# Kernel tuning notes

Hardware: AMD Instinct MI355X
Metric: run time of the kernel (lower is better)

Reference implementation:

```python
import jax, jax.numpy as jnp
import numpy as np

FRAMES = 31
FFT_LEN = 2048


def setup_inputs() -> dict:
    key = jax.random.key(0)
    ks = jax.random.split(key, 7)
    B = 1024
    x = jax.random.normal(ks[0], (B, FRAMES * FFT_LEN), dtype=jnp.float32)
    # torch nn.Linear params: weight [out, in], bias [out]
    def lin(k, fan_in, fan_out):
        bound = 1.0 / np.sqrt(fan_in)
        kw, kb = jax.random.split(k)
        W = jax.random.uniform(kw, (fan_out, fan_in), minval=-bound, maxval=bound, dtype=jnp.float32)
        b = jax.random.uniform(kb, (fan_out,), minval=-bound, maxval=bound, dtype=jnp.float32)
        return W, b
    W1, b1 = lin(ks[1], FFT_LEN, 256)
    W2, b2 = lin(ks[2], 256, 256)
    W3, b3 = lin(ks[3], 256, 1)
    return {"x": x, "W1": W1, "b1": b1, "W2": W2, "b2": b2, "W3": W3, "b3": b3}


def reference(x, W1, b1, W2, b2, W3, b3):
    B = x.shape[0]
    # flatten, take first 31*2048 elements, reshape, batched FFT along last axis
    xf = x.reshape(B, -1)[:, : FRAMES * FFT_LEN].reshape(B, FRAMES, FFT_LEN)
    spec = jnp.fft.fftn(xf, axes=(-1,))          # [B, 31, 2048] complex64
    spec_mean = jnp.mean(spec, axis=1)            # [B, 2048] complex64
    h = spec_mean.real.astype(jnp.float32)        # torch .type(FloatTensor) keeps real part
    h = jax.nn.relu(h @ W1.T + b1)
    h = jax.nn.relu(h @ W2.T + b2)
    out = jax.nn.sigmoid(h @ W3.T + b3)           # [B, 1]
    return out
```

## Files before the change

### kernel.cpp

```cpp
#include <hip/hip_runtime.h>
#include <math.h>

#define B 1024
#define FRAMES 31
#define NFFT 2048
#define NH 256
#define TWO_PI 6.28318530717958647692f

#define KSPLIT 16
#define KRANGE (NFFT / KSPLIT)
#define BT 32
#define JP 260
#define HP 36

__global__ __launch_bounds__(256) void k_mean_fft(const float* __restrict__ x,
                                                  float* __restrict__ h) {
    __shared__ float re[NFFT];
    __shared__ float im[NFFT];
    __shared__ float ct[NFFT];
    const int tid = threadIdx.x;
    const int b = blockIdx.x;
    const float* xr = x + (size_t)b * (FRAMES * NFFT);

#pragma unroll
    for (int s = 0; s < 8; ++s) {
        int i = tid + (s << 8);
        ct[i] = cosf(TWO_PI * (float)i / (float)NFFT);
    }

    float acc[8];
#pragma unroll
    for (int s = 0; s < 8; ++s) acc[s] = 0.f;
    for (int f = 0; f < FRAMES; ++f) {
        const float* fr = xr + f * NFFT;
#pragma unroll
        for (int s = 0; s < 8; ++s) acc[s] += fr[tid + (s << 8)];
    }
    const float inv = 1.0f / (float)FRAMES;
#pragma unroll
    for (int s = 0; s < 8; ++s) {
        int n = tid + (s << 8);
        int rv = __brev((unsigned)n) >> 21;
        re[rv] = acc[s] * inv;
        im[rv] = 0.f;
    }
    __syncthreads();

    for (int stage = 1; stage <= 11; ++stage) {
        const int half = 1 << (stage - 1);
        const int tsh = 11 - stage;
#pragma unroll
        for (int s = 0; s < 4; ++s) {
            int idx = tid + (s << 8);
            int j = idx & (half - 1);
            int base = ((idx >> (stage - 1)) << stage) + j;
            int ti = j << tsh;
            float wr = ct[ti];
            float wi = -ct[(ti + 1536) & (NFFT - 1)];
            float ar = re[base], ai = im[base];
            float br = re[base + half], bi = im[base + half];
            float tr = wr * br - wi * bi;
            float tq = wr * bi + wi * br;
            re[base] = ar + tr;
            im[base] = ai + tq;
            re[base + half] = ar - tr;
            im[base + half] = ai - tq;
        }
        __syncthreads();
    }

    float* hr = h + (size_t)b * NFFT;
#pragma unroll
    for (int s = 0; s < 8; ++s)
        hr[tid + (s << 8)] = re[tid + (s << 8)];
}

__global__ __launch_bounds__(256) void k_gemm1(const float* __restrict__ h,
                                               const float* __restrict__ W1,
                                               float* __restrict__ yp) {
    __shared__ float W1s[32 * JP];
    __shared__ float hs[32 * HP];
    const int tid = threadIdx.x;
    const int b0 = blockIdx.x * BT;
    const int kb0 = blockIdx.y * KRANGE;

    const int j0 = (tid & 63) * 4;
    const int bo = (tid >> 6) * 8;

    float acc[8][4];
#pragma unroll
    for (int i = 0; i < 8; ++i)
#pragma unroll
        for (int q = 0; q < 4; ++q) acc[i][q] = 0.f;

    for (int kc = 0; kc < KRANGE; kc += 32) {
        const int kb = kb0 + kc;
#pragma unroll
        for (int s = 0; s < 8; ++s) {
            int f = tid + (s << 8);
            int j = f >> 3;
            int k4 = f & 7;
            float4 v = *(const float4*)(W1 + (size_t)j * NFFT + kb + k4 * 4);
            W1s[(k4 * 4 + 0) * JP + j] = v.x;
            W1s[(k4 * 4 + 1) * JP + j] = v.y;
            W1s[(k4 * 4 + 2) * JP + j] = v.z;
            W1s[(k4 * 4 + 3) * JP + j] = v.w;
        }
        {
            int bb = tid >> 3;
            int k4 = tid & 7;
            float4 v = *(const float4*)(h + (size_t)(b0 + bb) * NFFT + kb + k4 * 4);
            hs[(k4 * 4 + 0) * HP + bb] = v.x;
            hs[(k4 * 4 + 1) * HP + bb] = v.y;
            hs[(k4 * 4 + 2) * HP + bb] = v.z;
            hs[(k4 * 4 + 3) * HP + bb] = v.w;
        }
        __syncthreads();

#pragma unroll 8
        for (int k = 0; k < 32; ++k) {
            float4 w = *(const float4*)&W1s[k * JP + j0];
            float4 hA = *(const float4*)&hs[k * HP + bo];
            float4 hB = *(const float4*)&hs[k * HP + bo + 4];
            acc[0][0] = fmaf(hA.x, w.x, acc[0][0]); acc[0][1] = fmaf(hA.x, w.y, acc[0][1]);
            acc[0][2] = fmaf(hA.x, w.z, acc[0][2]); acc[0][3] = fmaf(hA.x, w.w, acc[0][3]);
            acc[1][0] = fmaf(hA.y, w.x, acc[1][0]); acc[1][1] = fmaf(hA.y, w.y, acc[1][1]);
            acc[1][2] = fmaf(hA.y, w.z, acc[1][2]); acc[1][3] = fmaf(hA.y, w.w, acc[1][3]);
            acc[2][0] = fmaf(hA.z, w.x, acc[2][0]); acc[2][1] = fmaf(hA.z, w.y, acc[2][1]);
            acc[2][2] = fmaf(hA.z, w.z, acc[2][2]); acc[2][3] = fmaf(hA.z, w.w, acc[2][3]);
            acc[3][0] = fmaf(hA.w, w.x, acc[3][0]); acc[3][1] = fmaf(hA.w, w.y, acc[3][1]);
            acc[3][2] = fmaf(hA.w, w.z, acc[3][2]); acc[3][3] = fmaf(hA.w, w.w, acc[3][3]);
            acc[4][0] = fmaf(hB.x, w.x, acc[4][0]); acc[4][1] = fmaf(hB.x, w.y, acc[4][1]);
            acc[4][2] = fmaf(hB.x, w.z, acc[4][2]); acc[4][3] = fmaf(hB.x, w.w, acc[4][3]);
            acc[5][0] = fmaf(hB.y, w.x, acc[5][0]); acc[5][1] = fmaf(hB.y, w.y, acc[5][1]);
            acc[5][2] = fmaf(hB.y, w.z, acc[5][2]); acc[5][3] = fmaf(hB.y, w.w, acc[5][3]);
            acc[6][0] = fmaf(hB.z, w.x, acc[6][0]); acc[6][1] = fmaf(hB.z, w.y, acc[6][1]);
            acc[6][2] = fmaf(hB.z, w.z, acc[6][2]); acc[6][3] = fmaf(hB.z, w.w, acc[6][3]);
            acc[7][0] = fmaf(hB.w, w.x, acc[7][0]); acc[7][1] = fmaf(hB.w, w.y, acc[7][1]);
            acc[7][2] = fmaf(hB.w, w.z, acc[7][2]); acc[7][3] = fmaf(hB.w, w.w, acc[7][3]);
        }
        __syncthreads();
    }

    float* yo = yp + (size_t)blockIdx.y * (B * NH);
#pragma unroll
    for (int i = 0; i < 8; ++i) {
        float4 v = make_float4(acc[i][0], acc[i][1], acc[i][2], acc[i][3]);
        *(float4*)(yo + (size_t)(b0 + bo + i) * NH + j0) = v;
    }
}

__global__ __launch_bounds__(256) void k_reduce_relu(const float* __restrict__ yp,
                                                     const float* __restrict__ b1,
                                                     float* __restrict__ y1) {
    int f = blockIdx.x * 256 + threadIdx.x;
    const float4* p = (const float4*)yp;
    float4 a = p[f];
#pragma unroll
    for (int s = 1; s < KSPLIT; ++s) {
        float4 v = p[f + s * (B * NH / 4)];
        a.x += v.x; a.y += v.y; a.z += v.z; a.w += v.w;
    }
    float4 bb = ((const float4*)b1)[f & 63];
    a.x = fmaxf(a.x + bb.x, 0.f);
    a.y = fmaxf(a.y + bb.y, 0.f);
    a.z = fmaxf(a.z + bb.z, 0.f);
    a.w = fmaxf(a.w + bb.w, 0.f);
    ((float4*)y1)[f] = a;
}

__global__ __launch_bounds__(256) void k_head(const float* __restrict__ y1,
                                              const float* __restrict__ W2,
                                              const float* __restrict__ b2,
                                              const float* __restrict__ W3,
                                              const float* __restrict__ b3,
                                              float* __restrict__ out) {
    __shared__ float ys[4 * NH];
    __shared__ float red[4 * NH];
    const int tid = threadIdx.x;
    const int b0 = blockIdx.x * 4;
    ((float4*)ys)[tid] = ((const float4*)(y1 + (size_t)b0 * NH))[tid];
    __syncthreads();

    const float4* w2 = (const float4*)(W2 + (size_t)tid * NH);
    float a0 = 0.f, a1 = 0.f, a2 = 0.f, a3 = 0.f;
#pragma unroll 8
    for (int n4 = 0; n4 < NH / 4; ++n4) {
        float4 w = w2[n4];
        float4 v0 = ((const float4*)ys)[n4];
        float4 v1 = ((const float4*)ys)[64 + n4];
        float4 v2 = ((const float4*)ys)[128 + n4];
        float4 v3 = ((const float4*)ys)[192 + n4];
        a0 = fmaf(w.x, v0.x, a0); a0 = fmaf(w.y, v0.y, a0);
        a0 = fmaf(w.z, v0.z, a0); a0 = fmaf(w.w, v0.w, a0);
        a1 = fmaf(w.x, v1.x, a1); a1 = fmaf(w.y, v1.y, a1);
        a1 = fmaf(w.z, v1.z, a1); a1 = fmaf(w.w, v1.w, a1);
        a2 = fmaf(w.x, v2.x, a2); a2 = fmaf(w.y, v2.y, a2);
        a2 = fmaf(w.z, v2.z, a2); a2 = fmaf(w.w, v2.w, a2);
        a3 = fmaf(w.x, v3.x, a3); a3 = fmaf(w.y, v3.y, a3);
        a3 = fmaf(w.z, v3.z, a3); a3 = fmaf(w.w, v3.w, a3);
    }
    float w3 = W3[tid];
    float bb = b2[tid];
    red[tid]       = fmaxf(a0 + bb, 0.f) * w3;
    red[256 + tid] = fmaxf(a1 + bb, 0.f) * w3;
    red[512 + tid] = fmaxf(a2 + bb, 0.f) * w3;
    red[768 + tid] = fmaxf(a3 + bb, 0.f) * w3;
    __syncthreads();
    for (int s = 128; s > 0; s >>= 1) {
        if (tid < s) {
#pragma unroll
            for (int q = 0; q < 4; ++q)
                red[q * 256 + tid] += red[q * 256 + tid + s];
        }
        __syncthreads();
    }
    if (tid < 4)
        out[b0 + tid] = 1.f / (1.f + expf(-(red[tid * 256] + b3[0])));
}

extern "C" void kernel_launch(void* const* d_in, const int* in_sizes, int n_in,
                              void* d_out, int out_size, void* d_ws, size_t ws_size,
                              hipStream_t stream) {
    const float* x  = (const float*)d_in[0];
    const float* W1 = (const float*)d_in[1];
    const float* b1 = (const float*)d_in[2];
    const float* W2 = (const float*)d_in[3];
    const float* b2 = (const float*)d_in[4];
    const float* W3 = (const float*)d_in[5];
    const float* b3 = (const float*)d_in[6];
    float* out = (float*)d_out;

    char* ws = (char*)d_ws;
    float* h  = (float*)(ws);
    float* yp = (float*)(ws + (8u  << 20));
    float* y1 = (float*)(ws + (24u << 20));

    hipLaunchKernelGGL(k_mean_fft,    dim3(B),       dim3(256), 0, stream, x, h);
    hipLaunchKernelGGL(k_gemm1,       dim3(32, 16),  dim3(256), 0, stream, h, W1, yp);
    hipLaunchKernelGGL(k_reduce_relu, dim3(256),     dim3(256), 0, stream, yp, b1, y1);
    hipLaunchKernelGGL(k_head,        dim3(256),     dim3(256), 0, stream, y1, W2, b2, W3, b3, out);
}
```

Measured before the change: 426.9 us.

## Use real-FFT symmetry to halve FFT size and fold W1 columns

Exploits Hermitian symmetry of the real input's spectrum: a 1024-point complex FFT with a post-twiddle step produces the real part for bins 0..1023. W1 columns k and N-k are summed into a folded weight matrix, halving the GEMM K dimension, and the Nyquist bin is added separately in the tail. The reduce/ReLU kernel is merged into the head kernel, and W2 is staged through shared memory. It adds a small per-call weight-folding kernel, but the run is dominated by reading the large input x, which is unchanged.

Measured after the change: 427.3 us. About the same (+0.1%).

```diff
diff --git a/kernel.cpp b/kernel.cpp
--- a/kernel.cpp
+++ b/kernel.cpp
@@ -4,19 +4,34 @@
 #define B 1024
 #define FRAMES 31
 #define NFFT 2048
+#define NHALF 1024
 #define NH 256
 #define TWO_PI 6.28318530717958647692f
 
 #define KSPLIT 16
-#define KRANGE (NFFT / KSPLIT)
+#define KRANGE (NHALF / KSPLIT)
 #define BT 32
 #define JP 260
 #define HP 36
 
-__global__ __launch_bounds__(256) void k_mean_fft(const float* __restrict__ x,
-                                                  float* __restrict__ h) {
-    __shared__ float re[NFFT];
-    __shared__ float im[NFFT];
+__global__ __launch_bounds__(256) void k_fold(const float* __restrict__ W1,
+                                              float* __restrict__ Wf,
+                                              float* __restrict__ Wc) {
+    int idx = blockIdx.x * 256 + threadIdx.x;
+    int j = idx >> 10;
+    int k = idx & 1023;
+    float v = W1[(size_t)j * NFFT + k];
+    if (k) v += W1[(size_t)j * NFFT + (NFFT - k)];
+    Wf[idx] = v;
+    if (k == 0) Wc[j] = W1[(size_t)j * NFFT + 1024];
+}
+
+__global__ __launch_bounds__(256) void k_mean_rfft(const float* __restrict__ x,
+                                                   float* __restrict__ hh,
+                                                   float* __restrict__ h1024) {
+    __shared__ float xs[NFFT];
+    __shared__ float zr[NHALF];
+    __shared__ float zi[NHALF];
     __shared__ float ct[NFFT];
     const int tid = threadIdx.x;
     const int b = blockIdx.x;
@@ -38,47 +53,59 @@
     }
     const float inv = 1.0f / (float)FRAMES;
 #pragma unroll
-    for (int s = 0; s < 8; ++s) {
-        int n = tid + (s << 8);
-        int rv = __brev((unsigned)n) >> 21;
-        re[rv] = acc[s] * inv;
-        im[rv] = 0.f;
-    }
-    __syncthreads();
-
-    for (int stage = 1; stage <= 11; ++stage) {
-        const int half = 1 << (stage - 1);
-        const int tsh = 11 - stage;
-#pragma unroll
-        for (int s = 0; s < 4; ++s) {
+    for (int s = 0; s < 8; ++s) xs[tid + (s << 8)] = acc[s] * inv;
+    __syncthreads();
+
+#pragma unroll
+    for (int m = 0; m < 4; ++m) {
+        int n = tid + (m << 8);
+        int rv = __brev((unsigned)n) >> 22;
+        zr[rv] = xs[2 * n];
+        zi[rv] = xs[2 * n + 1];
+    }
+    __syncthreads();
+
+    for (int st = 1; st <= 10; ++st) {
+        const int half = 1 << (st - 1);
+        const int tsh = 11 - st;
+#pragma unroll
+        for (int s = 0; s < 2; ++s) {
             int idx = tid + (s << 8);
             int j = idx & (half - 1);
-            int base = ((idx >> (stage - 1)) << stage) + j;
+            int base = ((idx >> (st - 1)) << st) + j;
             int ti = j << tsh;
             float wr = ct[ti];
             float wi = -ct[(ti + 1536) & (NFFT - 1)];
-            float ar = re[base], ai = im[base];
-            float br = re[base + half], bi = im[base + half];
+            float ar = zr[base], ai = zi[base];
+            float br = zr[base + half], bi = zi[base + half];
             float tr = wr * br - wi * bi;
             float tq = wr * bi + wi * br;
-            re[base] = ar + tr;
-            im[base] = ai + tq;
-            re[base + half] = ar - tr;
-            im[base + half] = ai - tq;
-        }
-        __syncthreads();
-    }
-
-    float* hr = h + (size_t)b * NFFT;
-#pragma unroll
-    for (int s = 0; s < 8; ++s)
-        hr[tid + (s << 8)] = re[tid + (s << 8)];
-}
-
-__global__ __launch_bounds__(256) void k_gemm1(const float* __restrict__ h,
-                                               const float* __restrict__ W1,
+            zr[base] = ar + tr;
+            zi[base] = ai + tq;
+            zr[base + half] = ar - tr;
+            zi[base + half] = ai - tq;
+        }
+        __syncthreads();
+    }
+
+    float* ho = hh + (size_t)b * NHALF;
+#pragma unroll
+    for (int m = 0; m < 4; ++m) {
+        int k = tid + (m << 8);
+        int km = (NHALF - k) & (NHALF - 1);
+        float a = zr[k], bb = zi[k];
+        float c = zr[km], d = zi[km];
+        float cosv = ct[k];
+        float sinv = ct[(k + 1536) & (NFFT - 1)];
+        ho[k] = 0.5f * ((a + c) + cosv * (bb + d) - sinv * (a - c));
+    }
+    if (tid == 0) h1024[b] = zr[0] - zi[0];
+}
+
+__global__ __launch_bounds__(256) void k_gemm1(const float* __restrict__ hh,
+                                               const float* __restrict__ Wf,
                                                float* __restrict__ yp) {
-    __shared__ float W1s[32 * JP];
+    __shared__ float Ws[32 * JP];
     __shared__ float hs[32 * HP];
     const int tid = threadIdx.x;
     const int b0 = blockIdx.x * BT;
@@ -100,16 +127,16 @@
             int f = tid + (s << 8);
             int j = f >> 3;
             int k4 = f & 7;
-            float4 v = *(const float4*)(W1 + (size_t)j * NFFT + kb + k4 * 4);
-            W1s[(k4 * 4 + 0) * JP + j] = v.x;
-            W1s[(k4 * 4 + 1) * JP + j] = v.y;
-            W1s[(k4 * 4 + 2) * JP + j] = v.z;
-            W1s[(k4 * 4 + 3) * JP + j] = v.w;
+            float4 v = *(const float4*)(Wf + (size_t)j * NHALF + kb + k4 * 4);
+            Ws[(k4 * 4 + 0) * JP + j] = v.x;
+            Ws[(k4 * 4 + 1) * JP + j] = v.y;
+            Ws[(k4 * 4 + 2) * JP + j] = v.z;
+            Ws[(k4 * 4 + 3) * JP + j] = v.w;
         }
         {
             int bb = tid >> 3;
             int k4 = tid & 7;
-            float4 v = *(const float4*)(h + (size_t)(b0 + bb) * NFFT + kb + k4 * 4);
+            float4 v = *(const float4*)(hh + (size_t)(b0 + bb) * NHALF + kb + k4 * 4);
             hs[(k4 * 4 + 0) * HP + bb] = v.x;
             hs[(k4 * 4 + 1) * HP + bb] = v.y;
             hs[(k4 * 4 + 2) * HP + bb] = v.z;
@@ -119,7 +146,7 @@
 
 #pragma unroll 8
         for (int k = 0; k < 32; ++k) {
-            float4 w = *(const float4*)&W1s[k * JP + j0];
+            float4 w = *(const float4*)&Ws[k * JP + j0];
             float4 hA = *(const float4*)&hs[k * HP + bo];
             float4 hB = *(const float4*)&hs[k * HP + bo + 4];
             acc[0][0] = fmaf(hA.x, w.x, acc[0][0]); acc[0][1] = fmaf(hA.x, w.y, acc[0][1]);
@@ -150,73 +177,84 @@
     }
 }
 
-__global__ __launch_bounds__(256) void k_reduce_relu(const float* __restrict__ yp,
-                                                     const float* __restrict__ b1,
-                                                     float* __restrict__ y1) {
-    int f = blockIdx.x * 256 + threadIdx.x;
-    const float4* p = (const float4*)yp;
-    float4 a = p[f];
-#pragma unroll
-    for (int s = 1; s < KSPLIT; ++s) {
-        float4 v = p[f + s * (B * NH / 4)];
-        a.x += v.x; a.y += v.y; a.z += v.z; a.w += v.w;
-    }
-    float4 bb = ((const float4*)b1)[f & 63];
-    a.x = fmaxf(a.x + bb.x, 0.f);
-    a.y = fmaxf(a.y + bb.y, 0.f);
-    a.z = fmaxf(a.z + bb.z, 0.f);
-    a.w = fmaxf(a.w + bb.w, 0.f);
-    ((float4*)y1)[f] = a;
-}
-
-__global__ __launch_bounds__(256) void k_head(const float* __restrict__ y1,
+__global__ __launch_bounds__(256) void k_tail(const float* __restrict__ yp,
+                                              const float* __restrict__ b1,
+                                              const float* __restrict__ Wc,
+                                              const float* __restrict__ h1024,
                                               const float* __restrict__ W2,
                                               const float* __restrict__ b2,
                                               const float* __restrict__ W3,
                                               const float* __restrict__ b3,
                                               float* __restrict__ out) {
     __shared__ float ys[4 * NH];
+    __shared__ float w2s[NH * 36];
     __shared__ float red[4 * NH];
     const int tid = threadIdx.x;
     const int b0 = blockIdx.x * 4;
-    ((float4*)ys)[tid] = ((const float4*)(y1 + (size_t)b0 * NH))[tid];
-    __syncthreads();
-
-    const float4* w2 = (const float4*)(W2 + (size_t)tid * NH);
-    float a0 = 0.f, a1 = 0.f, a2 = 0.f, a3 = 0.f;
-#pragma unroll 8
-    for (int n4 = 0; n4 < NH / 4; ++n4) {
-        float4 w = w2[n4];
-        float4 v0 = ((const float4*)ys)[n4];
-        float4 v1 = ((const float4*)ys)[64 + n4];
-        float4 v2 = ((const float4*)ys)[128 + n4];
-        float4 v3 = ((const float4*)ys)[192 + n4];
-        a0 = fmaf(w.x, v0.x, a0); a0 = fmaf(w.y, v0.y, a0);
-        a0 = fmaf(w.z, v0.z, a0); a0 = fmaf(w.w, v0.w, a0);
-        a1 = fmaf(w.x, v1.x, a1); a1 = fmaf(w.y, v1.y, a1);
-        a1 = fmaf(w.z, v1.z, a1); a1 = fmaf(w.w, v1.w, a1);
-        a2 = fmaf(w.x, v2.x, a2); a2 = fmaf(w.y, v2.y, a2);
-        a2 = fmaf(w.z, v2.z, a2); a2 = fmaf(w.w, v2.w, a2);
-        a3 = fmaf(w.x, v3.x, a3); a3 = fmaf(w.y, v3.y, a3);
-        a3 = fmaf(w.z, v3.z, a3); a3 = fmaf(w.w, v3.w, a3);
-    }
+
+    {
+        int r = tid >> 6;
+        int j = (tid & 63) * 4;
+        const float* base = yp + (size_t)(b0 + r) * NH + j;
+        float4 a = *(const float4*)(base);
+#pragma unroll
+        for (int s = 1; s < KSPLIT; ++s) {
+            float4 v = *(const float4*)(base + (size_t)s * (B * NH));
+            a.x += v.x; a.y += v.y; a.z += v.z; a.w += v.w;
+        }
+        float4 bb = *(const float4*)(b1 + j);
+        float4 wc = *(const float4*)(Wc + j);
+        float hq = h1024[b0 + r];
+        a.x = fmaxf(a.x + bb.x + hq * wc.x, 0.f);
+        a.y = fmaxf(a.y + bb.y + hq * wc.y, 0.f);
+        a.z = fmaxf(a.z + bb.z + hq * wc.z, 0.f);
+        a.w = fmaxf(a.w + bb.w + hq * wc.w, 0.f);
+        *(float4*)(ys + r * NH + j) = a;
+    }
+    __syncthreads();
+
+    float a2[4] = {0.f, 0.f, 0.f, 0.f};
+    for (int kc = 0; kc < NH; kc += 32) {
+#pragma unroll
+        for (int s = 0; s < 8; ++s) {
+            int f = tid + (s << 8);
+            int j = f >> 3;
+            int k4 = f & 7;
+            float4 v = *(const float4*)(W2 + (size_t)j * NH + kc + k4 * 4);
+            *(float4*)(w2s + j * 36 + k4 * 4) = v;
+        }
+        __syncthreads();
+#pragma unroll
+        for (int k4 = 0; k4 < 8; ++k4) {
+            float4 w = *(const float4*)(w2s + tid * 36 + k4 * 4);
+#pragma unroll
+            for (int r = 0; r < 4; ++r) {
+                float4 y = *(const float4*)(ys + r * NH + kc + k4 * 4);
+                a2[r] = fmaf(w.x, y.x, a2[r]);
+                a2[r] = fmaf(w.y, y.y, a2[r]);
+                a2[r] = fmaf(w.z, y.z, a2[r]);
+                a2[r] = fmaf(w.w, y.w, a2[r]);
+            }
+        }
+        __syncthreads();
+    }
+
     float w3 = W3[tid];
-    float bb = b2[tid];
-    red[tid]       = fmaxf(a0 + bb, 0.f) * w3;
-    red[256 + tid] = fmaxf(a1 + bb, 0.f) * w3;
-    red[512 + tid] = fmaxf(a2 + bb, 0.f) * w3;
-    red[768 + tid] = fmaxf(a3 + bb, 0.f) * w3;
+    float bb2 = b2[tid];
+#pragma unroll
+    for (int r = 0; r < 4; ++r)
+        red[r * NH + tid] = fmaxf(a2[r] + bb2, 0.f) * w3;
     __syncthreads();
     for (int s = 128; s > 0; s >>= 1) {
         if (tid < s) {
 #pragma unroll
-            for (int q = 0; q < 4; ++q)
-                red[q * 256 + tid] += red[q * 256 + tid + s];
+            for (int r = 0; r < 4; ++r)
+                red[r * NH + tid] += red[r * NH + tid + s];
         }
         __syncthreads();
     }
     if (tid < 4)
-        out[b0 + tid] = 1.f / (1.f + expf(-(red[tid * 256] + b3[0])));
+        out[b0 + tid] = 1.f / (1.f + expf(-(red[tid * NH] + b3[0])));
 }
 
 extern "C" void kernel_launch(void* const* d_in, const int* in_sizes, int n_in,
@@ -232,12 +270,15 @@
     float* out = (float*)d_out;
 
     char* ws = (char*)d_ws;
-    float* h  = (float*)(ws);
-    float* yp = (float*)(ws + (8u  << 20));
-    float* y1 = (float*)(ws + (24u << 20));
-
-    hipLaunchKernelGGL(k_mean_fft,    dim3(B),       dim3(256), 0, stream, x, h);
-    hipLaunchKernelGGL(k_gemm1,       dim3(32, 16),  dim3(256), 0, stream, h, W1, yp);
-    hipLaunchKernelGGL(k_reduce_relu, dim3(256),     dim3(256), 0, stream, yp, b1, y1);
-    hipLaunchKernelGGL(k_head,        dim3(256),     dim3(256), 0, stream, y1, W2, b2, W3, b3, out);
-}
+    float* hh    = (float*)(ws);
+    float* yp    = (float*)(ws + (4u  << 20));
+    float* Wf    = (float*)(ws + (20u << 20));
+    float* Wc    = (float*)(ws + (21u << 20));
+    float* h1024 = (float*)(ws + (21u << 20) + 65536);
+
+    hipLaunchKernelGGL(k_fold,      dim3(1024),   dim3(256), 0, stream, W1, Wf, Wc);
+    hipLaunchKernelGGL(k_mean_rfft, dim3(B),      dim3(256), 0, stream, x, hh, h1024);
+    hipLaunchKernelGGL(k_gemm1,     dim3(32, 16), dim3(256), 0, stream, hh, Wf, yp);
+    hipLaunchKernelGGL(k_tail,      dim3(256),    dim3(256), 0, stream, yp, b1, Wc, h1024,
+                       W2, b2, W3, b3, out);
+}
```
